# Optimization experiments

Measured on AMD Instinct MI355X. Metric: run time of the kernel, lower is better.

Reference implementation:

```python
import jax, jax.numpy as jnp
import numpy as np

EXPAND = 2  # expand_ratio: head dim


def setup_inputs() -> dict:
    key = jax.random.key(0)
    k1, k2, k3 = jax.random.split(key, 3)
    n, b, d = 4096, 8, 1024
    x = jax.random.normal(k1, (n, b, d), dtype=jnp.float32)
    lower_bound = jnp.zeros((d,), dtype=jnp.float32)
    W_in = jax.random.normal(k2, (d, 3 * d), dtype=jnp.float32) / np.sqrt(d)
    W_out = jax.random.normal(k3, (d, d), dtype=jnp.float32) / np.sqrt(d)
    return {"x": x, "lower_bound": lower_bound, "W_in": W_in, "W_out": W_out}


def reference(x, lower_bound, W_in, W_out):
    # x: (n, b, d) sequence-first
    n, b, d = x.shape
    e = EXPAND
    h = d // e
    feat = x @ W_in                                  # (n, b, 3d)
    V, Q, Fg = jnp.split(feat, 3, axis=-1)
    V = jax.nn.gelu(V, approximate=False)            # nn.GELU default = exact erf
    Q = jax.nn.gelu(Q, approximate=False)
    Fg = jax.nn.sigmoid(Fg)
    V = V.reshape(n, b, h, e)
    Q = Q.reshape(n, b, h, e)
    Fg = Fg.reshape(n, b, h, e)
    lb = lower_bound.reshape(h, e)
    lam = lb + (1.0 - lb) * Fg                       # decay gate in (lb, 1)
    K = 1.0 - lam
    # GLA recurrence: S_t = diag(lam_t) S_{t-1} + k_t v_t^T ; o_t = q_t S_t
    # (exp(log_lambda) == lambda, so log-space decay collapses to direct multiply)
    def step(S, inp):
        lam_t, k_t, v_t, q_t = inp                   # each (b, h, e)
        S = lam_t[..., :, None] * S + k_t[..., :, None] * v_t[..., None, :]
        o_t = jnp.einsum('bhk,bhkv->bhv', q_t, S)
        return S, o_t
    S0 = jnp.zeros((b, h, e, e), dtype=x.dtype)
    _, o = jax.lax.scan(step, S0, (lam, K, V, Q))    # o: (n, b, h, e)
    o = o.reshape(n, b, d)
    return o @ W_out
```

## Files before the change

### kernel.cpp

```cpp
#include <hip/hip_runtime.h>
#include <hip/hip_bf16.h>
#include <math.h>

using frag8 = __attribute__((ext_vector_type(8))) short;
using f32x4 = __attribute__((ext_vector_type(4))) float;

#define BM 128
#define BN 128
#define BK 64

typedef const __attribute__((address_space(1))) unsigned char glb_u8;
typedef __attribute__((address_space(3))) unsigned char lds_u8;

__device__ __forceinline__ float b2f(unsigned short v) {
    union { unsigned u; float f; } x; x.u = ((unsigned)v) << 16; return x.f;
}
__device__ __forceinline__ unsigned short f2b(float f) {
    union { float f; unsigned u; } x; x.f = f;
    unsigned u = x.u;
    u += 0x7fffu + ((u >> 16) & 1u);
    return (unsigned short)(u >> 16);
}

__global__ __launch_bounds__(256) void cast_kernel(const float* __restrict__ in,
                                                   unsigned short* __restrict__ out, long n) {
    long i = ((long)blockIdx.x * 256 + threadIdx.x) * 8;
    if (i >= n) return;
    float4 a = *(const float4*)(in + i);
    float4 b = *(const float4*)(in + i + 4);
    struct alignas(16) U8 { unsigned short s[8]; } o;
    o.s[0] = f2b(a.x); o.s[1] = f2b(a.y); o.s[2] = f2b(a.z); o.s[3] = f2b(a.w);
    o.s[4] = f2b(b.x); o.s[5] = f2b(b.y); o.s[6] = f2b(b.z); o.s[7] = f2b(b.w);
    *(U8*)(out + i) = o;
}

__global__ void transpose_cast(const float* __restrict__ in, unsigned short* __restrict__ out,
                               int R, int Ccols) {
    __shared__ float tile[32][33];
    int bx = blockIdx.x * 32;
    int by = blockIdx.y * 32;
    int tx = threadIdx.x, ty = threadIdx.y;
    for (int r = ty; r < 32; r += 8)
        tile[r][tx] = in[(size_t)(by + r) * Ccols + bx + tx];
    __syncthreads();
    for (int r = ty; r < 32; r += 8)
        out[(size_t)(bx + r) * R + by + tx] = f2b(tile[tx][r]);
}

__global__ __launch_bounds__(256, 2) void gemm_bf16(
    const unsigned short* __restrict__ A, const unsigned short* __restrict__ Bt,
    int M, int N, int K, int mode,
    float* __restrict__ Cf,
    unsigned short* __restrict__ Vp, unsigned short* __restrict__ Qp,
    unsigned short* __restrict__ Lp, const float* __restrict__ lb) {
    __shared__ __align__(16) unsigned short sA[2 * BM * BK];
    __shared__ __align__(16) unsigned short sB[2 * BN * BK];
    const int tid = threadIdx.x;
    const int lane16 = tid & 15;
    const int quad = (tid & 63) >> 4;
    const int wave = tid >> 6;
    const int wm = (wave >> 1) * 64;
    const int wn = (wave & 1) * 64;

    const int MT = M / BM, NT = N / BN;
    const int bid = blockIdx.x;
    const int xcd = bid & 7;
    const int j = bid >> 3;
    const int mt = xcd * (MT >> 3) + j / NT;
    const int nt = j % NT;
    const long m0 = (long)mt * BM;
    const long n0 = (long)nt * BN;
    const long K2 = (long)K * 2;

    long srcAB[4];
    int ldsOff[4];
#pragma unroll
    for (int p = 0; p < 4; ++p) {
        int off = p * 4096 + tid * 16;
        int r = off >> 7;
        int c = (off >> 4) & 7;
        int sc = c ^ (r & 7);
        ldsOff[p] = off;
        srcAB[p] = (long)r * K2 + (long)sc * 16;
    }
    const char* Ab = (const char*)A + m0 * K2;
    const char* Bb = (const char*)Bt + n0 * K2;

    int ldsA[2][4], ldsB[2][4];
#pragma unroll
    for (int mf = 0; mf < 4; ++mf) {
        int rowA = wm + mf * 16 + lane16;
        int rowB = wn + mf * 16 + lane16;
#pragma unroll
        for (int ks = 0; ks < 2; ++ks) {
            int jj = quad + 4 * ks;
            ldsA[ks][mf] = rowA * 64 + ((jj ^ (rowA & 7)) * 8);
            ldsB[ks][mf] = rowB * 64 + ((jj ^ (rowB & 7)) * 8);
        }
    }

    f32x4 acc[4][4];
#pragma unroll
    for (int i = 0; i < 4; ++i)
#pragma unroll
        for (int jj = 0; jj < 4; ++jj) acc[i][jj] = (f32x4){0.f, 0.f, 0.f, 0.f};

    const int NIT = K / BK;
#pragma unroll
    for (int p = 0; p < 4; ++p) {
        __builtin_amdgcn_global_load_lds((glb_u8*)(Ab + srcAB[p]),
                                         (lds_u8*)((char*)sA + ldsOff[p]), 16, 0, 0);
        __builtin_amdgcn_global_load_lds((glb_u8*)(Bb + srcAB[p]),
                                         (lds_u8*)((char*)sB + ldsOff[p]), 16, 0, 0);
    }

    for (int it = 0; it < NIT; ++it) {
        __syncthreads();
        if (it + 1 < NIT) {
            long kb = (long)(it + 1) * BK * 2;
            int bo = ((it + 1) & 1) * 16384;
#pragma unroll
            for (int p = 0; p < 4; ++p) {
                __builtin_amdgcn_global_load_lds((glb_u8*)(Ab + srcAB[p] + kb),
                                                 (lds_u8*)((char*)sA + bo + ldsOff[p]), 16, 0, 0);
                __builtin_amdgcn_global_load_lds((glb_u8*)(Bb + srcAB[p] + kb),
                                                 (lds_u8*)((char*)sB + bo + ldsOff[p]), 16, 0, 0);
            }
        }
        const int bs = (it & 1) * 8192;
#pragma unroll
        for (int ks = 0; ks < 2; ++ks) {
            frag8 af[4], bfr[4];
#pragma unroll
            for (int mf = 0; mf < 4; ++mf) af[mf] = *(const frag8*)(sA + bs + ldsA[ks][mf]);
#pragma unroll
            for (int nf = 0; nf < 4; ++nf) bfr[nf] = *(const frag8*)(sB + bs + ldsB[ks][nf]);
#pragma unroll
            for (int mf = 0; mf < 4; ++mf)
#pragma unroll
                for (int nf = 0; nf < 4; ++nf)
                    acc[mf][nf] = __builtin_amdgcn_mfma_f32_16x16x32_bf16(af[mf], bfr[nf], acc[mf][nf], 0, 0, 0);
        }
    }

    if (mode == 0) {
#pragma unroll
        for (int mf = 0; mf < 4; ++mf)
#pragma unroll
            for (int nf = 0; nf < 4; ++nf) {
                long col = n0 + wn + nf * 16 + lane16;
#pragma unroll
                for (int r = 0; r < 4; ++r) {
                    long row = m0 + wm + mf * 16 + quad * 4 + r;
                    Cf[row * N + col] = acc[mf][nf][r];
                }
            }
    } else {
        const int seg = (int)(n0 >> 10);
        const int cbase = (int)(n0 & 1023) + wn;
        unsigned short* dst = (seg == 0) ? Vp : (seg == 1 ? Qp : Lp);
#pragma unroll
        for (int mf = 0; mf < 4; ++mf)
#pragma unroll
            for (int nf = 0; nf < 4; ++nf) {
                int col = cbase + nf * 16 + lane16;
#pragma unroll
                for (int r = 0; r < 4; ++r) {
                    long row = m0 + wm + mf * 16 + quad * 4 + r;
                    float v = acc[mf][nf][r];
                    float res;
                    if (seg < 2) {
                        float u = 1.59576912f * v * (1.0f + 0.044715f * v * v);
                        res = v / (1.0f + __expf(-u));
                    } else {
                        float sg = 1.0f / (1.0f + __expf(-v));
                        float l = lb[col];
                        res = l + (1.0f - l) * sg;
                    }
                    dst[row * 1024 + col] = f2b(res);
                }
            }
    }
}

__global__ __launch_bounds__(256) void scan_phase1(
    const unsigned short* __restrict__ lam, const unsigned short* __restrict__ V,
    float* __restrict__ Sl, float* __restrict__ P, int L) {
    int cid = blockIdx.x * 256 + threadIdx.x;
    int c = blockIdx.y;
    int bi = cid >> 9, h = cid & 511;
    float s00 = 0, s01 = 0, s10 = 0, s11 = 0, p0 = 1.f, p1 = 1.f;
    int t0 = c * L;
    const unsigned* lamp = (const unsigned*)lam;
    const unsigned* vp = (const unsigned*)V;
    for (int t = t0; t < t0 + L; ++t) {
        long idx = (long)(t * 8 + bi) * 512 + h;
        unsigned lu = lamp[idx], vu = vp[idx];
        float la0 = b2f((unsigned short)lu), la1 = b2f((unsigned short)(lu >> 16));
        float v0 = b2f((unsigned short)vu), v1 = b2f((unsigned short)(vu >> 16));
        float k0 = 1.f - la0, k1 = 1.f - la1;
        s00 = fmaf(la0, s00, k0 * v0); s01 = fmaf(la0, s01, k0 * v1);
        s10 = fmaf(la1, s10, k1 * v0); s11 = fmaf(la1, s11, k1 * v1);
        p0 *= la0; p1 *= la1;
    }
    long base = (long)c * 4096 + cid;
    ((float4*)Sl)[base] = make_float4(s00, s01, s10, s11);
    ((float2*)P)[base] = make_float2(p0, p1);
}

__global__ __launch_bounds__(256) void scan_phase2(
    const float* __restrict__ Sl, const float* __restrict__ P,
    float* __restrict__ Sini, int C) {
    int idx = blockIdx.x * 256 + threadIdx.x;
    int cid = idx >> 2, ij = idx & 3, i = (idx >> 1) & 1;
    float s = 0.f;
    for (int c = 0; c < C; ++c) {
        long base = (long)c * 4096 + cid;
        Sini[base * 4 + ij] = s;
        s = fmaf(P[base * 2 + i], s, Sl[base * 4 + ij]);
    }
}

__global__ __launch_bounds__(256) void scan_phase3(
    const unsigned short* __restrict__ lam, const unsigned short* __restrict__ V,
    const unsigned short* __restrict__ Q, const float* __restrict__ Sini,
    unsigned short* __restrict__ o, int L) {
    int cid = blockIdx.x * 256 + threadIdx.x;
    int c = blockIdx.y;
    int bi = cid >> 9, h = cid & 511;
    float4 si = ((const float4*)Sini)[(long)c * 4096 + cid];
    float s00 = si.x, s01 = si.y, s10 = si.z, s11 = si.w;
    int t0 = c * L;
    const unsigned* lamp = (const unsigned*)lam;
    const unsigned* vp = (const unsigned*)V;
    const unsigned* qp = (const unsigned*)Q;
    unsigned* op = (unsigned*)o;
    for (int t = t0; t < t0 + L; ++t) {
        long idx = (long)(t * 8 + bi) * 512 + h;
        unsigned lu = lamp[idx], vu = vp[idx], qu = qp[idx];
        float la0 = b2f((unsigned short)lu), la1 = b2f((unsigned short)(lu >> 16));
        float v0 = b2f((unsigned short)vu), v1 = b2f((unsigned short)(vu >> 16));
        float q0 = b2f((unsigned short)qu), q1 = b2f((unsigned short)(qu >> 16));
        float k0 = 1.f - la0, k1 = 1.f - la1;
        s00 = fmaf(la0, s00, k0 * v0); s01 = fmaf(la0, s01, k0 * v1);
        s10 = fmaf(la1, s10, k1 * v0); s11 = fmaf(la1, s11, k1 * v1);
        float o0 = q0 * s00 + q1 * s10;
        float o1 = q0 * s01 + q1 * s11;
        op[idx] = (unsigned)f2b(o0) | ((unsigned)f2b(o1) << 16);
    }
}

extern "C" void kernel_launch(void* const* d_in, const int* in_sizes, int n_in,
                              void* d_out, int out_size, void* d_ws, size_t ws_size,
                              hipStream_t stream) {
    const float* x = (const float*)d_in[0];
    const float* lb = (const float*)d_in[1];
    const float* W_in = (const float*)d_in[2];
    const float* W_out = (const float*)d_in[3];
    float* out = (float*)d_out;

    const int n = 4096, b = 8, d = 1024;
    const long NB = (long)n * b;
    const int C = 64, L = 64;

    char* ws = (char*)d_ws;
    size_t off = 0;
    auto alloc = [&](size_t bytes) -> char* {
        char* p = ws + off;
        off += (bytes + 255) & ~(size_t)255;
        return p;
    };
    unsigned short* xb   = (unsigned short*)alloc(NB * d * 2);
    unsigned short* Wint = (unsigned short*)alloc((size_t)3 * d * d * 2);
    unsigned short* Wot  = (unsigned short*)alloc((size_t)d * d * 2);
    unsigned short* Vb   = (unsigned short*)alloc(NB * d * 2);
    unsigned short* Qb   = (unsigned short*)alloc(NB * d * 2);
    unsigned short* Lb   = (unsigned short*)alloc(NB * d * 2);
    float* Sl   = (float*)alloc((size_t)C * 4096 * 4 * 4);
    float* P    = (float*)alloc((size_t)C * 4096 * 2 * 4);
    float* Sini = (float*)alloc((size_t)C * 4096 * 4 * 4);

    cast_kernel<<<dim3((unsigned)((NB * d) / (256 * 8))), 256, 0, stream>>>(x, xb, NB * d);
    transpose_cast<<<dim3(3 * d / 32, d / 32), dim3(32, 8), 0, stream>>>(W_in, Wint, d, 3 * d);
    transpose_cast<<<dim3(d / 32, d / 32), dim3(32, 8), 0, stream>>>(W_out, Wot, d, d);
    gemm_bf16<<<dim3((unsigned)((NB / BM) * (3 * d / BN))), 256, 0, stream>>>(
        xb, Wint, (int)NB, 3 * d, d, 1, nullptr, Vb, Qb, Lb, lb);
    scan_phase1<<<dim3(16, C), 256, 0, stream>>>(Lb, Vb, Sl, P, L);
    scan_phase2<<<dim3(64), 256, 0, stream>>>(Sl, P, Sini, C);
    unsigned short* ob = xb;
    scan_phase3<<<dim3(16, C), 256, 0, stream>>>(Lb, Vb, Qb, Sini, ob, L);
    gemm_bf16<<<dim3((unsigned)((NB / BM) * (d / BN))), 256, 0, stream>>>(
        ob, Wot, (int)NB, d, d, 0, out, nullptr, nullptr, nullptr, nullptr);
}
```

Baseline: 793.9 us.

## Load GEMM B fragments directly from global memory, drop B LDS staging

The GEMM now stages only the A tile in shared memory and has each wave read its B (weight) fragments straight from global memory into registers each K step. Halving LDS use lets the launch bound rise to three blocks per CU. The XCD-aware tile swizzle is replaced by a plain 2D grid. The risk is that B reads are no longer shared across the waves of a block and are not prefetched, so global-load latency lands directly before the MFMAs and L2 locality across XCDs may get worse.

```diff
diff --git a/kernel.cpp b/kernel.cpp
--- a/kernel.cpp
+++ b/kernel.cpp
@@ -47,32 +47,24 @@
         out[(size_t)(bx + r) * R + by + tx] = f2b(tile[tx][r]);
 }
 
-__global__ __launch_bounds__(256, 2) void gemm_bf16(
+__global__ __launch_bounds__(256, 3) void gemm_bf16(
     const unsigned short* __restrict__ A, const unsigned short* __restrict__ Bt,
     int M, int N, int K, int mode,
     float* __restrict__ Cf,
     unsigned short* __restrict__ Vp, unsigned short* __restrict__ Qp,
     unsigned short* __restrict__ Lp, const float* __restrict__ lb) {
     __shared__ __align__(16) unsigned short sA[2 * BM * BK];
-    __shared__ __align__(16) unsigned short sB[2 * BN * BK];
     const int tid = threadIdx.x;
     const int lane16 = tid & 15;
     const int quad = (tid & 63) >> 4;
     const int wave = tid >> 6;
     const int wm = (wave >> 1) * 64;
     const int wn = (wave & 1) * 64;
-
-    const int MT = M / BM, NT = N / BN;
-    const int bid = blockIdx.x;
-    const int xcd = bid & 7;
-    const int j = bid >> 3;
-    const int mt = xcd * (MT >> 3) + j / NT;
-    const int nt = j % NT;
-    const long m0 = (long)mt * BM;
-    const long n0 = (long)nt * BN;
+    const long m0 = (long)blockIdx.x * BM;
+    const long n0 = (long)blockIdx.y * BN;
     const long K2 = (long)K * 2;
 
-    long srcAB[4];
+    long srcA[4];
     int ldsOff[4];
 #pragma unroll
     for (int p = 0; p < 4; ++p) {
@@ -81,21 +73,23 @@
         int c = (off >> 4) & 7;
         int sc = c ^ (r & 7);
         ldsOff[p] = off;
-        srcAB[p] = (long)r * K2 + (long)sc * 16;
+        srcA[p] = (long)r * K2 + (long)sc * 16;
     }
     const char* Ab = (const char*)A + m0 * K2;
-    const char* Bb = (const char*)Bt + n0 * K2;
-
-    int ldsA[2][4], ldsB[2][4];
+
+    const unsigned short* Brow[4];
+#pragma unroll
+    for (int nf = 0; nf < 4; ++nf)
+        Brow[nf] = Bt + (n0 + wn + nf * 16 + lane16) * (long)K + quad * 8;
+
+    int ldsA[2][4];
 #pragma unroll
     for (int mf = 0; mf < 4; ++mf) {
         int rowA = wm + mf * 16 + lane16;
-        int rowB = wn + mf * 16 + lane16;
 #pragma unroll
         for (int ks = 0; ks < 2; ++ks) {
             int jj = quad + 4 * ks;
             ldsA[ks][mf] = rowA * 64 + ((jj ^ (rowA & 7)) * 8);
-            ldsB[ks][mf] = rowB * 64 + ((jj ^ (rowB & 7)) * 8);
         }
     }
 
@@ -107,12 +101,9 @@
 
     const int NIT = K / BK;
 #pragma unroll
-    for (int p = 0; p < 4; ++p) {
-        __builtin_amdgcn_global_load_lds((glb_u8*)(Ab + srcAB[p]),
+    for (int p = 0; p < 4; ++p)
+        __builtin_amdgcn_global_load_lds((glb_u8*)(Ab + srcA[p]),
                                          (lds_u8*)((char*)sA + ldsOff[p]), 16, 0, 0);
-        __builtin_amdgcn_global_load_lds((glb_u8*)(Bb + srcAB[p]),
-                                         (lds_u8*)((char*)sB + ldsOff[p]), 16, 0, 0);
-    }
 
     for (int it = 0; it < NIT; ++it) {
         __syncthreads();
@@ -120,26 +111,30 @@
             long kb = (long)(it + 1) * BK * 2;
             int bo = ((it + 1) & 1) * 16384;
 #pragma unroll
-            for (int p = 0; p < 4; ++p) {
-                __builtin_amdgcn_global_load_lds((glb_u8*)(Ab + srcAB[p] + kb),
+            for (int p = 0; p < 4; ++p)
+                __builtin_amdgcn_global_load_lds((glb_u8*)(Ab + srcA[p] + kb),
                                                  (lds_u8*)((char*)sA + bo + ldsOff[p]), 16, 0, 0);
-                __builtin_amdgcn_global_load_lds((glb_u8*)(Bb + srcAB[p] + kb),
-                                                 (lds_u8*)((char*)sB + bo + ldsOff[p]), 16, 0, 0);
-            }
+        }
+        frag8 bfr[2][4];
+        {
+            const int kt = it * BK;
+#pragma unroll
+            for (int ks = 0; ks < 2; ++ks)
+#pragma unroll
+                for (int nf = 0; nf < 4; ++nf)
+                    bfr[ks][nf] = *(const frag8*)(Brow[nf] + kt + ks * 32);
         }
         const int bs = (it & 1) * 8192;
 #pragma unroll
         for (int ks = 0; ks < 2; ++ks) {
-            frag8 af[4], bfr[4];
+            frag8 af[4];
 #pragma unroll
             for (int mf = 0; mf < 4; ++mf) af[mf] = *(const frag8*)(sA + bs + ldsA[ks][mf]);
 #pragma unroll
-            for (int nf = 0; nf < 4; ++nf) bfr[nf] = *(const frag8*)(sB + bs + ldsB[ks][nf]);
-#pragma unroll
             for (int mf = 0; mf < 4; ++mf)
 #pragma unroll
                 for (int nf = 0; nf < 4; ++nf)
-                    acc[mf][nf] = __builtin_amdgcn_mfma_f32_16x16x32_bf16(af[mf], bfr[nf], acc[mf][nf], 0, 0, 0);
+                    acc[mf][nf] = __builtin_amdgcn_mfma_f32_16x16x32_bf16(af[mf], bfr[ks][nf], acc[mf][nf], 0, 0, 0);
         }
     }
 
@@ -283,12 +278,12 @@
     cast_kernel<<<dim3((unsigned)((NB * d) / (256 * 8))), 256, 0, stream>>>(x, xb, NB * d);
     transpose_cast<<<dim3(3 * d / 32, d / 32), dim3(32, 8), 0, stream>>>(W_in, Wint, d, 3 * d);
     transpose_cast<<<dim3(d / 32, d / 32), dim3(32, 8), 0, stream>>>(W_out, Wot, d, d);
-    gemm_bf16<<<dim3((unsigned)((NB / BM) * (3 * d / BN))), 256, 0, stream>>>(
+    gemm_bf16<<<dim3((unsigned)(NB / BM), 3 * d / BN), 256, 0, stream>>>(
         xb, Wint, (int)NB, 3 * d, d, 1, nullptr, Vb, Qb, Lb, lb);
     scan_phase1<<<dim3(16, C), 256, 0, stream>>>(Lb, Vb, Sl, P, L);
     scan_phase2<<<dim3(64), 256, 0, stream>>>(Sl, P, Sini, C);
     unsigned short* ob = xb;
     scan_phase3<<<dim3(16, C), 256, 0, stream>>>(Lb, Vb, Qb, Sini, ob, L);
-    gemm_bf16<<<dim3((unsigned)((NB / BM) * (d / BN))), 256, 0, stream>>>(
+    gemm_bf16<<<dim3((unsigned)(NB / BM), d / BN), 256, 0, stream>>>(
         ob, Wot, (int)NB, d, d, 0, out, nullptr, nullptr, nullptr, nullptr);
 }
```

Result: slower. 938.0 us (+18.2%).
